# Kernel optimization log

Hardware: AMD Instinct MI355X
Metric: run time of the kernel (lower is better)

The kernel has to match this reference:

```python
import jax, jax.numpy as jnp
import numpy as np

B = 1
H_IMG, W_IMG = 64, 64
NF = H_IMG * W_IMG          # 4096 front/query tokens
NS = 1024                   # satellite tokens (32x32 grid)
SAT_IN, FRONT_IN = 768, 320
NH, HD = 8, 64
MD = NH * HD                # 512
GHID, GHD = 128, 16
GMD = NH * GHD              # 128
GEO_RATIO, ROPE_BASE = 0.5, 10000.0
LAMBDA_GEO, LAMBDA_GEOM = 1.0, 1.0
EPS = 1e-5


def _linear(x, w, b):
    return x @ w.T + b


def _layernorm(x, g, b):
    m = x.mean(-1, keepdims=True)
    v = jnp.var(x, axis=-1, keepdims=True)
    return (x - m) / jnp.sqrt(v + EPS) * g + b


def _georope(t, xy):
    """Continuous 2D (x,y) rotary embedding on the first GEO_RATIO fraction of head_dim.
    t: [B,NH,N,HD], xy: [B,N,2]."""
    rot = int(HD * GEO_RATIO)       # rotated dims (32)
    axis = rot // 2                 # dims per spatial axis (16)
    half = axis // 2                # frequency pairs per axis (8)
    inv_freq = ROPE_BASE ** (-jnp.arange(half, dtype=t.dtype) / half)

    def rot_axis(a, coord):
        th = coord[:, None, :, None] * inv_freq   # [B,1,N,half]
        c, s = jnp.cos(th), jnp.sin(th)
        a1, a2 = a[..., :half], a[..., half:]
        return jnp.concatenate([a1 * c - a2 * s, a1 * s + a2 * c], axis=-1)

    tx = rot_axis(t[..., :axis], xy[..., 0])
    ty = rot_axis(t[..., axis:rot], xy[..., 1])
    return jnp.concatenate([tx, ty, t[..., rot:]], axis=-1)


def _heads(x, hd):
    b, n, _ = x.shape
    return x.reshape(b, n, NH, hd).transpose(0, 2, 1, 3)


def setup_inputs() -> dict:
    key = jax.random.key(0)
    ks = iter(jax.random.split(key, 64))

    def w(*shape):
        return jax.random.normal(next(ks), shape, jnp.float32) / np.sqrt(shape[-1]).astype(np.float32)

    z = lambda n: jnp.zeros((n,), jnp.float32)
    o = lambda n: jnp.ones((n,), jnp.float32)
    return {
        "front_feat": jax.random.normal(next(ks), (B, FRONT_IN, H_IMG, W_IMG), jnp.float32),
        "front_bev_xy": jax.random.uniform(next(ks), (B, NF, 2), jnp.float32, -1.0, 1.0),
        "sat_tokens": jax.random.normal(next(ks), (B, NS, SAT_IN), jnp.float32),
        "sat_xy": jax.random.uniform(next(ks), (B, NS, 2), jnp.float32, -1.0, 1.0),
        "front_plucker": jax.random.normal(next(ks), (B, NF, 6), jnp.float32),
        "pos_w1": w(MD, 2), "pos_b1": z(MD), "pos_w2": w(MD, MD), "pos_b2": z(MD),
        "fa_w": w(MD, FRONT_IN), "fa_b": z(MD), "fa_ln_g": o(MD), "fa_ln_b": z(MD),
        "qn_g": o(MD), "qn_b": z(MD),
        "sa_w": w(MD, SAT_IN), "sa_b": z(MD), "sa_ln_g": o(MD), "sa_ln_b": z(MD),
        "wq": w(MD, MD), "bq": z(MD), "wk": w(MD, MD), "bk": z(MD), "wv": w(MD, MD), "bv": z(MD),
        "plk_w1": w(GHID, 6), "plk_b1": z(GHID), "plk_w2": w(GHID, GHID), "plk_b2": z(GHID),
        "sxy_w1": w(GHID, 2), "sxy_b1": z(GHID), "sxy_w2": w(GHID, GHID), "sxy_b2": z(GHID),
        "gqn_g": o(GHID), "gqn_b": z(GHID), "gkn_g": o(GHID), "gkn_b": z(GHID),
        "wqg": w(GMD, GHID), "bqg": z(GMD), "wkg": w(GMD, GHID), "bkg": z(GMD),
    }


def reference(front_feat, front_bev_xy, sat_tokens, sat_xy, front_plucker,
              pos_w1, pos_b1, pos_w2, pos_b2, fa_w, fa_b, fa_ln_g, fa_ln_b,
              qn_g, qn_b, sa_w, sa_b, sa_ln_g, sa_ln_b, wq, bq, wk, bk, wv, bv,
              plk_w1, plk_b1, plk_w2, plk_b2, sxy_w1, sxy_b1, sxy_w2, sxy_b2,
              gqn_g, gqn_b, gkn_g, gkn_b, wqg, bqg, wkg, bkg):
    b = front_feat.shape[0]
    ff = front_feat.reshape(b, FRONT_IN, NF).transpose(0, 2, 1)      # [B,NF,C]
    pos = _linear(jax.nn.silu(_linear(front_bev_xy, pos_w1, pos_b1)), pos_w2, pos_b2)
    feat = _layernorm(_linear(ff, fa_w, fa_b), fa_ln_g, fa_ln_b)
    q_embed = _layernorm(pos + feat, qn_g, qn_b)
    sat_feat = _layernorm(_linear(sat_tokens, sa_w, sa_b), sa_ln_g, sa_ln_b)
    q = _heads(_linear(q_embed, wq, bq), HD)                         # [B,H,NF,HD]
    k = _heads(_linear(sat_feat, wk, bk), HD)                        # [B,H,NS,HD]
    v = _heads(_linear(sat_feat, wv, bv), HD)
    qr = _georope(q, front_bev_xy)
    kr = _georope(k, sat_xy)
    logits = jnp.einsum('bhqd,bhkd->bhqk', qr, kr) / np.float32(np.sqrt(HD))
    # learned geometric Q/K stream (Plucker rays vs sat xy)
    plk = _layernorm(_linear(jax.nn.silu(_linear(front_plucker, plk_w1, plk_b1)), plk_w2, plk_b2), gqn_g, gqn_b)
    sgf = _layernorm(_linear(jax.nn.silu(_linear(sat_xy, sxy_w1, sxy_b1)), sxy_w2, sxy_b2), gkn_g, gkn_b)
    qg = _heads(_linear(plk, wqg, bqg), GHD)
    kg = _heads(_linear(sgf, wkg, bkg), GHD)
    logits = logits + LAMBDA_GEOM * (jnp.einsum('bhqd,bhkd->bhqk', qg, kg) / np.float32(np.sqrt(GHD)))
    # additive pairwise squared-distance bias, broadcast over heads
    dist2 = ((front_bev_xy[:, :, None, :] - sat_xy[:, None, :, :]) ** 2).sum(-1)   # [B,NF,NS]
    logits = logits - LAMBDA_GEO * dist2[:, None]
    attn = jax.nn.softmax(logits, axis=-1)
    read = jnp.einsum('bhqk,bhkd->bhqd', attn, v)
    return read.transpose(0, 2, 1, 3).reshape(b, NF, MD)
```

## Files before the change

kernel.cpp:

```cpp
#include <hip/hip_runtime.h>
#include <hip/hip_bf16.h>
#include <stdint.h>

#define NF 4096
#define NS 1024
#define MD 512
#define HD 64
#define DA 96
#define GHID 128

#define L2E 1.44269504f
#define S2L 1.6986436f
#define SMAX 12.0f

typedef unsigned short u16;
typedef __attribute__((ext_vector_type(8))) short bf8v;
typedef __attribute__((ext_vector_type(4))) float f4v;

__device__ __forceinline__ u16 f2bf(float f) {
  __hip_bfloat16 h = __float2bfloat16(f);
  return __builtin_bit_cast(u16, h);
}
__device__ __forceinline__ float bf2f(u16 u) {
  union { unsigned u; float f; } v; v.u = ((unsigned)u) << 16; return v.f;
}
__device__ __forceinline__ f4v mfma16(bf8v a, bf8v b, f4v c) {
  return __builtin_amdgcn_mfma_f32_16x16x32_bf16(a, b, c, 0, 0, 0);
}
__device__ __forceinline__ void gld16(const void* g, void* l) {
  __builtin_amdgcn_global_load_lds(
      (const __attribute__((address_space(1))) unsigned int*)g,
      (__attribute__((address_space(3))) unsigned int*)l, 16, 0, 0);
}

#define OFF_POSW2 0
#define OFF_FAW   262144
#define OFF_SAW   425984
#define OFF_WQ    819200
#define OFF_WKV   1081344
#define OFF_PLKW2 1605632
#define OFF_SXYW2 1622016
#define OFF_WQG   1638400
#define OFF_WKG   1654784
#define OFF_SATT  1671168
#define TOTW      2457600

#define EPI_OUT  0
#define EPI_ROPE 1
#define EPI_VT   2
#define EPI_GEO  3

__global__ __launch_bounds__(256) void k_l0(
    const float* __restrict__ s0, const float* __restrict__ s1,
    const float* __restrict__ s2, const float* __restrict__ s3,
    const float* __restrict__ s4, const float* __restrict__ s5,
    const float* __restrict__ s6, const float* __restrict__ s7,
    const float* __restrict__ s8, const float* __restrict__ s9,
    const float* __restrict__ s10, u16* __restrict__ pool,
    const float* __restrict__ bk, const float* __restrict__ bv,
    float* __restrict__ bkv,
    const float* __restrict__ ff, u16* __restrict__ ffT,
    const float* __restrict__ in0, const float* __restrict__ w0,
    const float* __restrict__ b0, u16* __restrict__ o0,
    const float* __restrict__ in1, const float* __restrict__ w1,
    const float* __restrict__ b1, u16* __restrict__ o1,
    const float* __restrict__ in2, const float* __restrict__ w2,
    const float* __restrict__ b2, u16* __restrict__ o2,
    u16* __restrict__ Qaug, u16* __restrict__ Kaug, float* __restrict__ kk2) {
  __shared__ u16 sT[32][72];
  int blk = blockIdx.x, t = threadIdx.x;
  if (blk < 2401) {
    int i4 = blk * 256 + t;
    if (i4 < TOTW / 4) {
      int idx = i4 * 4;
      const float* src; int off;
      if      (idx < OFF_FAW)   { src = s0;  off = OFF_POSW2; }
      else if (idx < OFF_SAW)   { src = s1;  off = OFF_FAW; }
      else if (idx < OFF_WQ)    { src = s2;  off = OFF_SAW; }
      else if (idx < OFF_WKV)   { src = s3;  off = OFF_WQ; }
      else if (idx < 1343488)   { src = s4;  off = OFF_WKV; }
      else if (idx < OFF_PLKW2) { src = s5;  off = 1343488; }
      else if (idx < OFF_SXYW2) { src = s6;  off = OFF_PLKW2; }
      else if (idx < OFF_WQG)   { src = s7;  off = OFF_SXYW2; }
      else if (idx < OFF_WKG)   { src = s8;  off = OFF_WQG; }
      else if (idx < OFF_SATT)  { src = s9;  off = OFF_WKG; }
      else                      { src = s10; off = OFF_SATT; }
      float4 v = *(const float4*)(src + (idx - off));
      ushort4 o;
      o.x = f2bf(v.x); o.y = f2bf(v.y); o.z = f2bf(v.z); o.w = f2bf(v.w);
      *(ushort4*)(pool + idx) = o;
    } else if (i4 < TOTW / 4 + 256) {
      int j = (i4 - TOTW / 4) * 4;
#pragma unroll
      for (int e = 0; e < 4; ++e) {
        int b = j + e;
        bkv[b] = (b < 512) ? bk[b] : bv[b - 512];
      }
    }
  } else if (blk < 3041) {
    int lb = blk - 2401;
    int n0 = (lb & 63) * 64, c0 = (lb >> 6) * 32;
    {
      int cr = t >> 3, nc = (t & 7) * 8;
      const float* src = ff + (size_t)(c0 + cr) * NF + n0 + nc;
      float4 v0 = *(const float4*)src, v1 = *(const float4*)(src + 4);
      bf8v p;
      p[0]=(short)f2bf(v0.x); p[1]=(short)f2bf(v0.y); p[2]=(short)f2bf(v0.z); p[3]=(short)f2bf(v0.w);
      p[4]=(short)f2bf(v1.x); p[5]=(short)f2bf(v1.y); p[6]=(short)f2bf(v1.z); p[7]=(short)f2bf(v1.w);
      *(bf8v*)&sT[cr][nc] = p;
    }
    __syncthreads();
    {
      int r = t >> 2, cc = (t & 3) * 8;
      bf8v p;
#pragma unroll
      for (int e = 0; e < 8; ++e) p[e] = (short)sT[cc + e][r];
      *(bf8v*)(ffT + (size_t)(n0 + r) * 320 + c0 + cc) = p;
    }
  } else if (blk < 13793) {
    int lb = blk - 3041;
    const float *in, *w, *b; u16* o; int mlog, K, idx;
    if (lb < 8192)       { in = in0; w = w0; b = b0; o = o0; mlog = 9; K = 2; idx = lb * 256 + t; }
    else if (lb < 10240) { in = in1; w = w1; b = b1; o = o1; mlog = 7; K = 6; idx = (lb - 8192) * 256 + t; }
    else                 { in = in2; w = w2; b = b2; o = o2; mlog = 7; K = 2; idx = (lb - 10240) * 256 + t; }
    int M = 1 << mlog;
    int n = idx >> mlog, m = idx & (M - 1);
    float acc = b[m];
    for (int k = 0; k < K; ++k) acc += in[n * K + k] * w[m * K + k];
    o[idx] = f2bf(acc / (1.f + __expf(-acc)));
  } else {
    int id = (blk - 13793) * 256 + t;
    int side = id >= NF * 8;
    int lid = side ? id - NF * 8 : id;
    int n = lid >> 3, h = lid & 7;
    const float* xy = side ? in2 : in0;
    u16* aug = side ? Kaug : Qaug;
    int nrows = side ? NS : NF;
    float x = xy[n * 2], y = xy[n * 2 + 1];
    bf8v p0, z;
#pragma unroll
    for (int e = 0; e < 8; ++e) { p0[e] = 0; z[e] = 0; }
    p0[0] = (short)f2bf(S2L * x);
    p0[1] = (short)f2bf(S2L * y);
    u16* dst = aug + ((size_t)h * nrows + n) * DA + 80;
    *(bf8v*)dst = p0;
    *(bf8v*)(dst + 8) = z;
    if (side && h == 0) kk2[n] = L2E * (x * x + y * y) + SMAX;
  }
}

__device__ __forceinline__ void gemm_body128(const u16* __restrict__ A, const u16* __restrict__ W,
                                             const float* __restrict__ bias, u16* __restrict__ out,
                                             int m0, int n0, int N, int K) {
  __shared__ u16 sA[2][128 * 64];
  __shared__ u16 sB[2][64 * 64];
  const int tid = threadIdx.x, w = tid >> 6, lane = tid & 63;
  const int l16 = lane & 15, lh = lane >> 4;

  f4v acc[2][4];
#pragma unroll
  for (int m = 0; m < 2; ++m)
#pragma unroll
    for (int j = 0; j < 4; ++j) acc[m][j] = (f4v){0.f, 0.f, 0.f, 0.f};

  auto stageA = [&](int buf, int k0) {
#pragma unroll
    for (int i = 0; i < 4; ++i) {
      int c = i * 256 + tid;
      int row = c >> 3, cp = c & 7;
      int sc_ = cp ^ (row & 7);
      gld16(A + (size_t)(m0 + row) * K + k0 + sc_ * 8, &sA[buf][c * 8]);
    }
  };
  auto stageB = [&](int buf, int k0) {
#pragma unroll
    for (int i = 0; i < 2; ++i) {
      int c = i * 256 + tid;
      int row = c >> 3, cp = c & 7;
      int sc_ = cp ^ (row & 7);
      gld16(W + (size_t)(n0 + row) * K + k0 + sc_ * 8, &sB[buf][c * 8]);
    }
  };

  stageA(0, 0); stageB(0, 0);
  __syncthreads();
  const int NK = K >> 6;
  for (int ks = 0; ks < NK; ++ks) {
    int nb = ks & 1;
    if (ks + 1 < NK) { stageA(nb ^ 1, (ks + 1) * 64); stageB(nb ^ 1, (ks + 1) * 64); }
#pragma unroll
    for (int kk = 0; kk < 2; ++kk) {
      bf8v af[2], bfr[4];
#pragma unroll
      for (int m = 0; m < 2; ++m) {
        int row = w * 32 + m * 16 + l16;
        int cp = (kk * 4 + lh) ^ (row & 7);
        af[m] = *(const bf8v*)&sA[nb][row * 64 + cp * 8];
      }
#pragma unroll
      for (int j = 0; j < 4; ++j) {
        int row = j * 16 + l16;
        int cp = (kk * 4 + lh) ^ (row & 7);
        bfr[j] = *(const bf8v*)&sB[nb][row * 64 + cp * 8];
      }
#pragma unroll
      for (int m = 0; m < 2; ++m)
#pragma unroll
        for (int j = 0; j < 4; ++j) acc[m][j] = mfma16(af[m], bfr[j], acc[m][j]);
    }
    __syncthreads();
  }
#pragma unroll
  for (int m = 0; m < 2; ++m) {
    int grow = m0 + w * 32 + m * 16 + (lh << 2);
#pragma unroll
    for (int j = 0; j < 4; ++j) {
      int gcol = n0 + j * 16 + l16;
      float bvs = bias ? bias[gcol] : 0.f;
#pragma unroll
      for (int r = 0; r < 4; ++r)
        out[(size_t)(grow + r) * N + gcol] = f2bf(acc[m][j][r] + bvs);
    }
  }
}

__device__ __forceinline__ void gemm_body(const u16* __restrict__ A, const u16* __restrict__ W,
                                          const float* __restrict__ bias, u16* __restrict__ out,
                                          int m0, int n0, int N, int K,
                                          int mode, float scale, const float* __restrict__ xy,
                                          u16* __restrict__ aug, int nrows) {
  constexpr int MR = 2, NR = 2;
  __shared__ u16 sA[2][64 * 64];
  __shared__ u16 sB[2][64 * 64];
  const int tid = threadIdx.x, w = tid >> 6, lane = tid & 63;
  const int l16 = lane & 15, lh = lane >> 4;
  const int wr = w >> 1, wc = w & 1;

  f4v acc[MR][NR];
#pragma unroll
  for (int m = 0; m < MR; ++m)
#pragma unroll
    for (int j = 0; j < NR; ++j) acc[m][j] = (f4v){0.f, 0.f, 0.f, 0.f};

  auto stageA = [&](int buf, int k0) {
#pragma unroll
    for (int i = 0; i < 2; ++i) {
      int c = i * 256 + tid;
      int row = c >> 3, cp = c & 7;
      int sc_ = cp ^ (row & 7);
      gld16(A + (size_t)(m0 + row) * K + k0 + sc_ * 8, &sA[buf][c * 8]);
    }
  };
  auto stageB = [&](int buf, int k0) {
#pragma unroll
    for (int i = 0; i < 2; ++i) {
      int c = i * 256 + tid;
      int row = c >> 3, cp = c & 7;
      int sc_ = cp ^ (row & 7);
      gld16(W + (size_t)(n0 + row) * K + k0 + sc_ * 8, &sB[buf][c * 8]);
    }
  };

  stageA(0, 0); stageB(0, 0);
  __syncthreads();
  const int NK = K >> 6;
  for (int ks = 0; ks < NK; ++ks) {
    int nb = ks & 1;
    if (ks + 1 < NK) { stageA(nb ^ 1, (ks + 1) * 64); stageB(nb ^ 1, (ks + 1) * 64); }
#pragma unroll
    for (int kk = 0; kk < 2; ++kk) {
      bf8v af[MR], bfr[NR];
#pragma unroll
      for (int m = 0; m < MR; ++m) {
        int row = wr * 32 + m * 16 + l16;
        int cp = (kk * 4 + lh) ^ (row & 7);
        af[m] = *(const bf8v*)&sA[nb][row * 64 + cp * 8];
      }
#pragma unroll
      for (int j = 0; j < NR; ++j) {
        int row = wc * 32 + j * 16 + l16;
        int cp = (kk * 4 + lh) ^ (row & 7);
        bfr[j] = *(const bf8v*)&sB[nb][row * 64 + cp * 8];
      }
#pragma unroll
      for (int m = 0; m < MR; ++m)
#pragma unroll
        for (int j = 0; j < NR; ++j) acc[m][j] = mfma16(af[m], bfr[j], acc[m][j]);
    }
    __syncthreads();
  }

  if (mode == EPI_OUT) {
#pragma unroll
    for (int m = 0; m < MR; ++m) {
      int grow = m0 + wr * 32 + m * 16 + (lh << 2);
#pragma unroll
      for (int j = 0; j < NR; ++j) {
        int gcol = n0 + wc * 32 + j * 16 + l16;
        float bvs = bias ? bias[gcol] : 0.f;
#pragma unroll
        for (int r = 0; r < 4; ++r)
          out[(size_t)(grow + r) * N + gcol] = f2bf(acc[m][j][r] + bvs);
      }
    }
  } else if (mode == EPI_ROPE) {
    float fr = __expf(-(float)(l16 & 7) * 1.1512925465f);
#pragma unroll
    for (int m = 0; m < MR; ++m) {
      int grow = m0 + wr * 32 + m * 16 + (lh << 2);
#pragma unroll
      for (int j = 0; j < NR; ++j) {
        int gcol = n0 + wc * 32 + j * 16 + l16;
        int h = gcol >> 6, d = gcol & 63;
        float bvs = bias[gcol];
#pragma unroll
        for (int r = 0; r < 4; ++r) {
          int n = grow + r;
          float val = acc[m][j][r] + bvs;
          float part = __shfl_xor(val, 8);
          float outv = val;
          if (wc == 0) {
            float2 c2 = ((const float2*)xy)[n];
            float coord = j ? c2.y : c2.x;
            float sn, cs;
            __sincosf(coord * fr, &sn, &cs);
            outv = (l16 & 8) ? (part * sn + val * cs) : (val * cs - part * sn);
          }
          aug[((size_t)h * nrows + n) * DA + d] = f2bf(outv * scale);
        }
      }
    }
  } else if (mode == EPI_VT) {
#pragma unroll
    for (int m = 0; m < MR; ++m) {
      int grow = m0 + wr * 32 + m * 16 + (lh << 2);
#pragma unroll
      for (int j = 0; j < NR; ++j) {
        int gcol = n0 + wc * 32 + j * 16 + l16;
        int vcol = gcol - 512;
        int h = vcol >> 6, d = vcol & 63;
        float bvs = bias[gcol];
        ushort4 o;
        o.x = f2bf(acc[m][j][0] + bvs);
        o.y = f2bf(acc[m][j][1] + bvs);
        o.z = f2bf(acc[m][j][2] + bvs);
        o.w = f2bf(acc[m][j][3] + bvs);
        *(ushort4*)(aug + ((size_t)(h * 64 + d)) * NS + grow) = o;
      }
    }
  } else {
#pragma unroll
    for (int m = 0; m < MR; ++m) {
      int grow = m0 + wr * 32 + m * 16 + (lh << 2);
#pragma unroll
      for (int j = 0; j < NR; ++j) {
        int gcol = n0 + wc * 32 + j * 16 + l16;
        int h = gcol >> 4, dg = gcol & 15;
        float bvs = bias[gcol];
#pragma unroll
        for (int r = 0; r < 4; ++r)
          aug[((size_t)h * nrows + grow + r) * DA + 64 + dg] = f2bf((acc[m][j][r] + bvs) * scale);
      }
    }
  }
}

struct GP { const u16* A; const u16* W; const float* bias; u16* out;
            int K; int N; int M; int mode; float scale; const float* xy;
            u16* aug; int nrows; };

__device__ __forceinline__ void gemm_dispatch128(const GP& g, int blk) {
  int mt = g.M >> 7;
  int m0 = (blk % mt) * 128, n0 = (blk / mt) * 64;
  gemm_body128(g.A, g.W, g.bias, g.out, m0, n0, g.N, g.K);
}
__device__ __forceinline__ void gemm_dispatch(const GP& g, int blk) {
  int mt = g.M >> 6;
  int m0 = (blk % mt) * 64, n0 = (blk / mt) * 64;
  gemm_body(g.A, g.W, g.bias, g.out, m0, n0, g.N, g.K,
            g.mode, g.scale, g.xy, g.aug, g.nrows);
}

__global__ __launch_bounds__(256) void k_gemm_L1(GP a, GP b, GP c, GP d, GP e) {
  int blk = blockIdx.x;
  if (blk < 256)       gemm_dispatch128(a, blk);
  else if (blk < 512)  gemm_dispatch128(b, blk - 256);
  else if (blk < 576)  gemm_dispatch128(c, blk - 512);
  else if (blk < 640)  gemm_dispatch128(d, blk - 576);
  else                 gemm_dispatch128(e, blk - 640);
}
__global__ __launch_bounds__(256) void k_gemm_L2(GP a, GP b, GP c, GP d, u16* VTp) {
  int blk = blockIdx.x;
  if (blk < 512) {
    gemm_dispatch(a, blk);
  } else if (blk < 768) {
    int lb = blk - 512;
    int m0 = (lb & 15) * 64, n0 = (lb >> 4) * 64;
    if (n0 >= 512)
      gemm_body(b.A, b.W, b.bias, b.out, m0, n0, b.N, b.K, EPI_VT, 1.f, nullptr, VTp, NS);
    else
      gemm_body(b.A, b.W, b.bias, b.out, m0, n0, b.N, b.K, b.mode, b.scale, b.xy, b.aug, b.nrows);
  } else if (blk < 896) {
    gemm_dispatch(c, blk - 768);
  } else {
    gemm_dispatch(d, blk - 896);
  }
}

__global__ __launch_bounds__(256) void k_ln_all(
    const u16* __restrict__ feat_pre, const u16* __restrict__ pos,
    const float* __restrict__ fg, const float* __restrict__ fb,
    const float* __restrict__ qg, const float* __restrict__ qb2,
    u16* __restrict__ q_embed,
    const u16* __restrict__ satf_pre, const float* __restrict__ sg,
    const float* __restrict__ sb, u16* __restrict__ satf,
    const u16* __restrict__ ginq, const u16* __restrict__ gink,
    const float* __restrict__ ggq, const float* __restrict__ gbq,
    const float* __restrict__ ggk, const float* __restrict__ gbk,
    u16* __restrict__ goutq, u16* __restrict__ goutk) {
  int blk = blockIdx.x;
  int w = threadIdx.x >> 6, lane = threadIdx.x & 63;
  if (blk < 1024) {
    int row = blk * 4 + w;
    bf8v v = *(const bf8v*)(feat_pre + (size_t)row * 512 + lane * 8);
    float x[8];
#pragma unroll
    for (int e = 0; e < 8; ++e) x[e] = bf2f((u16)v[e]);
    float s = 0.f, q = 0.f;
#pragma unroll
    for (int e = 0; e < 8; ++e) { s += x[e]; q += x[e] * x[e]; }
#pragma unroll
    for (int mm = 1; mm < 64; mm <<= 1) { s += __shfl_xor(s, mm); q += __shfl_xor(q, mm); }
    float mean = s / 512.f, var = q / 512.f - mean * mean;
    float rstd = rsqrtf(var + 1e-5f);
    bf8v vp = *(const bf8v*)(pos + (size_t)row * 512 + lane * 8);
#pragma unroll
    for (int e = 0; e < 8; ++e)
      x[e] = (x[e] - mean) * rstd * fg[lane * 8 + e] + fb[lane * 8 + e] + bf2f((u16)vp[e]);
    s = 0.f; q = 0.f;
#pragma unroll
    for (int e = 0; e < 8; ++e) { s += x[e]; q += x[e] * x[e]; }
#pragma unroll
    for (int mm = 1; mm < 64; mm <<= 1) { s += __shfl_xor(s, mm); q += __shfl_xor(q, mm); }
    mean = s / 512.f; var = q / 512.f - mean * mean;
    rstd = rsqrtf(var + 1e-5f);
    bf8v ov;
#pragma unroll
    for (int e = 0; e < 8; ++e)
      ov[e] = (short)f2bf((x[e] - mean) * rstd * qg[lane * 8 + e] + qb2[lane * 8 + e]);
    *(bf8v*)(q_embed + (size_t)row * 512 + lane * 8) = ov;
  } else if (blk < 1280) {
    int row = (blk - 1024) * 4 + w;
    bf8v v = *(const bf8v*)(satf_pre + (size_t)row * 512 + lane * 8);
    float x[8];
#pragma unroll
    for (int e = 0; e < 8; ++e) x[e] = bf2f((u16)v[e]);
    float s = 0.f, q = 0.f;
#pragma unroll
    for (int e = 0; e < 8; ++e) { s += x[e]; q += x[e] * x[e]; }
#pragma unroll
    for (int mm = 1; mm < 64; mm <<= 1) { s += __shfl_xor(s, mm); q += __shfl_xor(q, mm); }
    float mean = s / 512.f, var = q / 512.f - mean * mean;
    float rstd = rsqrtf(var + 1e-5f);
    bf8v ov;
#pragma unroll
    for (int e = 0; e < 8; ++e)
      ov[e] = (short)f2bf((x[e] - mean) * rstd * sg[lane * 8 + e] + sb[lane * 8 + e]);
    *(bf8v*)(satf + (size_t)row * 512 + lane * 8) = ov;
  } else {
    int row = (blk - 1280) * 4 + w;
    const u16* in; const float *g, *b; u16* out;
    if (row < 4096) { in = ginq; g = ggq; b = gbq; out = goutq; }
    else { row -= 4096; in = gink; g = ggk; b = gbk; out = goutk; }
    uint32_t v = *(const uint32_t*)(in + (size_t)row * 128 + lane * 2);
    float x0 = bf2f((u16)(v & 0xffff)), x1 = bf2f((u16)(v >> 16));
    float s = x0 + x1, q = x0 * x0 + x1 * x1;
#pragma unroll
    for (int mm = 1; mm < 64; mm <<= 1) { s += __shfl_xor(s, mm); q += __shfl_xor(q, mm); }
    float mean = s / 128.f, var = q / 128.f - mean * mean;
    float rstd = rsqrtf(var + 1e-5f);
    u16 o0 = f2bf((x0 - mean) * rstd * g[lane * 2] + b[lane * 2]);
    u16 o1 = f2bf((x1 - mean) * rstd * g[lane * 2 + 1] + b[lane * 2 + 1]);
    *(uint32_t*)(out + (size_t)row * 128 + lane * 2) = (uint32_t)o0 | ((uint32_t)o1 << 16);
  }
}

__global__ __launch_bounds__(256, 5) void k_flash(const u16* __restrict__ Qa,
                                                  const u16* __restrict__ Ka,
                                                  const u16* __restrict__ VT,
                                                  const float* __restrict__ kk2,
                                                  u16* __restrict__ Opart,
                                                  float* __restrict__ lbuf) {
  const int h = blockIdx.y, qb = blockIdx.x, sp = blockIdx.z;
  const int tid = threadIdx.x, w = tid >> 6, lane = tid & 63;
  const int l16 = lane & 15, lh = lane >> 4;
  __shared__ u16 sK[64][100];
  __shared__ u16 sV[64][68];
  __shared__ u16 sP[4][16][68];
  __shared__ float sKK[512];

  ((float2*)sKK)[tid] = ((const float2*)(kk2 + sp * 512))[tid];

  const int qrow = qb * 64 + w * 16 + l16;
  bf8v qf[3];
#pragma unroll
  for (int c = 0; c < 3; ++c)
    qf[c] = *(const bf8v*)(Qa + (size_t)(h * NF + qrow) * DA + c * 32 + lh * 8);

  bf8v ONES;
#pragma unroll
  for (int i = 0; i < 8; ++i) ONES[i] = (short)0x3F80;

  const int crow = qb * 64 + w * 16 + (lh << 2);
  float l_run[4] = {0.f, 0.f, 0.f, 0.f};
  f4v accO[4];
#pragma unroll
  for (int d = 0; d < 4; ++d) accO[d] = (f4v){0.f, 0.f, 0.f, 0.f};

  const int kt0 = sp * 8;
  bf8v kreg[3], vreg[2];
  auto sload = [&](int t8) {
    int kb = (kt0 + t8) * 64;
#pragma unroll
    for (int i = 0; i < 3; ++i) {
      int c = tid + i * 256; int r = c / 12, off = (c % 12) * 8;
      kreg[i] = *(const bf8v*)(Ka + ((size_t)(h * NS) + kb + r) * DA + off);
    }
#pragma unroll
    for (int i = 0; i < 2; ++i) {
      int c = tid + i * 256; int d = c >> 3, off = (c & 7) * 8;
      vreg[i] = *(const bf8v*)(VT + ((size_t)(h * HD) + d) * NS + kb + off);
    }
  };
  auto swrite = [&]() {
#pragma unroll
    for (int i = 0; i < 3; ++i) {
      int c = tid + i * 256; int r = c / 12, off = (c % 12) * 8;
      *(bf8v*)&sK[r][off] = kreg[i];
    }
#pragma unroll
    for (int i = 0; i < 2; ++i) {
      int c = tid + i * 256; int d = c >> 3, off = (c & 7) * 8;
      *(bf8v*)&sV[d][off] = vreg[i];
    }
  };

  sload(0); swrite();
  __syncthreads();
  for (int t8 = 0; t8 < 8; ++t8) {
    if (t8 < 7) sload(t8 + 1);
#pragma unroll
    for (int j = 0; j < 4; ++j) {
      f4v s4 = (f4v){0.f, 0.f, 0.f, 0.f};
#pragma unroll
      for (int c = 0; c < 3; ++c) {
        bf8v kf = *(const bf8v*)&sK[j * 16 + l16][c * 32 + lh * 8];
        s4 = mfma16(qf[c], kf, s4);
      }
      float ck = sKK[t8 * 64 + j * 16 + l16];
#pragma unroll
      for (int r = 0; r < 4; ++r) {
        float pv = exp2f(s4[r] - ck);
        sP[w][(lh << 2) + r][j * 16 + l16] = f2bf(pv);
      }
    }
    bf8v pf0 = *(const bf8v*)&sP[w][l16][lh * 8];
    bf8v pf1 = *(const bf8v*)&sP[w][l16][32 + lh * 8];
    f4v ls = (f4v){0.f, 0.f, 0.f, 0.f};
    ls = mfma16(pf0, ONES, ls);
    ls = mfma16(pf1, ONES, ls);
#pragma unroll
    for (int r = 0; r < 4; ++r) l_run[r] += ls[r];
#pragma unroll
    for (int c = 0; c < 2; ++c) {
      bf8v pf = (c == 0) ? pf0 : pf1;
#pragma unroll
      for (int d = 0; d < 4; ++d) {
        bf8v vf = *(const bf8v*)&sV[d * 16 + l16][c * 32 + lh * 8];
        accO[d] = mfma16(pf, vf, accO[d]);
      }
    }
    __syncthreads();
    if (t8 < 7) swrite();
    __syncthreads();
  }
  size_t obase = (size_t)(sp * 8 + h) * NF + crow;
#pragma unroll
  for (int d = 0; d < 4; ++d)
#pragma unroll
    for (int r = 0; r < 4; ++r)
      Opart[(obase + r) * 64 + d * 16 + l16] = f2bf(accO[d][r]);
  if (l16 == 0) {
#pragma unroll
    for (int r = 0; r < 4; ++r) lbuf[obase + r] = l_run[r];
  }
}

__global__ void k_combine(const u16* __restrict__ Opart, const float* __restrict__ lbuf,
                          float* __restrict__ out) {
  int i4 = blockIdx.x * 256 + threadIdx.x;
  int n = i4 >> 7;
  int c4 = i4 & 127, h = c4 >> 4, d4 = c4 & 15;
  float l = lbuf[(size_t)h * NF + n] + lbuf[(size_t)(8 + h) * NF + n];
  float rl = 1.f / l;
  ushort4 a = ((const ushort4*)(Opart + ((size_t)h * NF + n) * 64))[d4];
  ushort4 b = ((const ushort4*)(Opart + ((size_t)(8 + h) * NF + n) * 64))[d4];
  float4 r;
  r.x = (bf2f(a.x) + bf2f(b.x)) * rl;
  r.y = (bf2f(a.y) + bf2f(b.y)) * rl;
  r.z = (bf2f(a.z) + bf2f(b.z)) * rl;
  r.w = (bf2f(a.w) + bf2f(b.w)) * rl;
  ((float4*)out)[i4] = r;
}

extern "C" void kernel_launch(void* const* d_in, const int* in_sizes, int n_in,
                              void* d_out, int out_size, void* d_ws, size_t ws_size,
                              hipStream_t stream) {
  (void)in_sizes; (void)n_in; (void)out_size; (void)ws_size;
  const float* front_feat = (const float*)d_in[0];
  const float* bev_xy     = (const float*)d_in[1];
  const float* sat_tokens = (const float*)d_in[2];
  const float* sat_xy     = (const float*)d_in[3];
  const float* plucker    = (const float*)d_in[4];
  const float* pos_w1 = (const float*)d_in[5];
  const float* pos_b1 = (const float*)d_in[6];
  const float* pos_w2 = (const float*)d_in[7];
  const float* pos_b2 = (const float*)d_in[8];
  const float* fa_w   = (const float*)d_in[9];
  const float* fa_b   = (const float*)d_in[10];
  const float* fa_ln_g = (const float*)d_in[11];
  const float* fa_ln_b = (const float*)d_in[12];
  const float* qn_g   = (const float*)d_in[13];
  const float* qn_b   = (const float*)d_in[14];
  const float* sa_w   = (const float*)d_in[15];
  const float* sa_b   = (const float*)d_in[16];
  const float* sa_ln_g = (const float*)d_in[17];
  const float* sa_ln_b = (const float*)d_in[18];
  const float* wq = (const float*)d_in[19];
  const float* bq = (const float*)d_in[20];
  const float* wk = (const float*)d_in[21];
  const float* bk = (const float*)d_in[22];
  const float* wv = (const float*)d_in[23];
  const float* bv = (const float*)d_in[24];
  const float* plk_w1 = (const float*)d_in[25];
  const float* plk_b1 = (const float*)d_in[26];
  const float* plk_w2 = (const float*)d_in[27];
  const float* plk_b2 = (const float*)d_in[28];
  const float* sxy_w1 = (const float*)d_in[29];
  const float* sxy_b1 = (const float*)d_in[30];
  const float* sxy_w2 = (const float*)d_in[31];
  const float* sxy_b2 = (const float*)d_in[32];
  const float* gqn_g = (const float*)d_in[33];
  const float* gqn_b = (const float*)d_in[34];
  const float* gkn_g = (const float*)d_in[35];
  const float* gkn_b = (const float*)d_in[36];
  const float* wqg = (const float*)d_in[37];
  const float* bqg = (const float*)d_in[38];
  const float* wkg = (const float*)d_in[39];
  const float* bkg = (const float*)d_in[40];

  char* ws = (char*)d_ws;
  size_t off = 0;
  auto alloc = [&](size_t bytes) {
    size_t r = off;
    off += (bytes + 255) & ~(size_t)255;
    return r;
  };
  u16*   wpool   = (u16*)(ws + alloc((size_t)TOTW * 2));
  float* bkv     = (float*)(ws + alloc(1024 * 4));
  u16*   ffT     = (u16*)(ws + alloc((size_t)NF * 320 * 2));
  u16*   pos_h   = (u16*)(ws + alloc((size_t)NF * MD * 2));
  u16*   plk_h   = (u16*)(ws + alloc((size_t)NF * GHID * 2));
  u16*   sxy_h   = (u16*)(ws + alloc((size_t)NS * GHID * 2));
  u16*   pos     = (u16*)(ws + alloc((size_t)NF * MD * 2));
  u16*   feat_pre= (u16*)(ws + alloc((size_t)NF * MD * 2));
  u16*   satf_pre= (u16*)(ws + alloc((size_t)NS * MD * 2));
  u16*   satf    = (u16*)(ws + alloc((size_t)NS * MD * 2));
  u16*   q_embed = (u16*)(ws + alloc((size_t)NF * MD * 2));
  u16*   plk2    = (u16*)(ws + alloc((size_t)NF * GHID * 2));
  u16*   sxy2    = (u16*)(ws + alloc((size_t)NS * GHID * 2));
  u16*   Qaug    = (u16*)(ws + alloc((size_t)8 * NF * DA * 2));
  u16*   Kaug    = (u16*)(ws + alloc((size_t)8 * NS * DA * 2));
  u16*   VT      = (u16*)(ws + alloc((size_t)8 * HD * NS * 2));
  float* kk2     = (float*)(ws + alloc((size_t)NS * 4));
  u16*   Opart   = (u16*)(ws + alloc((size_t)2 * 8 * NF * 64 * 2));
  float* lbuf    = (float*)(ws + alloc((size_t)2 * 8 * NF * 4));
  u16* plk_ln = plk_h;
  u16* sgf    = sxy_h;

  dim3 b256(256);
  k_l0<<<dim3(13953), b256, 0, stream>>>(
      pos_w2, fa_w, sa_w, wq, wk, wv, plk_w2, sxy_w2, wqg, wkg, sat_tokens,
      wpool, bk, bv, bkv, front_feat, ffT,
      bev_xy, pos_w1, pos_b1, pos_h,
      plucker, plk_w1, plk_b1, plk_h,
      sat_xy, sxy_w1, sxy_b1, sxy_h,
      Qaug, Kaug, kk2);

  GP gpos {pos_h, wpool + OFF_POSW2, pos_b2, pos, 512, 512, 4096, EPI_OUT, 0.f, nullptr, nullptr, 0};
  GP gfeat{ffT, wpool + OFF_FAW, fa_b, feat_pre, 320, 512, 4096, EPI_OUT, 0.f, nullptr, nullptr, 0};
  GP gsat {wpool + OFF_SATT, wpool + OFF_SAW, sa_b, satf_pre, 768, 512, 1024, EPI_OUT, 0.f, nullptr, nullptr, 0};
  GP ggq1 {plk_h, wpool + OFF_PLKW2, plk_b2, plk2, 128, 128, 4096, EPI_OUT, 0.f, nullptr, nullptr, 0};
  GP ggk1 {sxy_h, wpool + OFF_SXYW2, sxy_b2, sxy2, 128, 128, 1024, EPI_OUT, 0.f, nullptr, nullptr, 0};
  k_gemm_L1<<<dim3(656), b256, 0, stream>>>(gpos, gfeat, gsat, ggq1, ggk1);

  k_ln_all<<<dim3(2560), b256, 0, stream>>>(
      feat_pre, pos, fa_ln_g, fa_ln_b, qn_g, qn_b, q_embed,
      satf_pre, sa_ln_g, sa_ln_b, satf,
      plk2, sxy2, gqn_g, gqn_b, gkn_g, gkn_b, plk_ln, sgf);

  GP gq  {q_embed, wpool + OFF_WQ, bq, nullptr, 512, 512, 4096, EPI_ROPE, 0.125f * L2E, bev_xy, Qaug, NF};
  GP gkv {satf, wpool + OFF_WKV, bkv, nullptr, 512, 1024, 1024, EPI_ROPE, 1.f, sat_xy, Kaug, NS};
  GP ggq2{plk_ln, wpool + OFF_WQG, bqg, nullptr, 128, 128, 4096, EPI_GEO, 0.25f * L2E, nullptr, Qaug, NF};
  GP ggk2{sgf, wpool + OFF_WKG, bkg, nullptr, 128, 128, 1024, EPI_GEO, 1.f, nullptr, Kaug, NS};
  k_gemm_L2<<<dim3(928), b256, 0, stream>>>(gq, gkv, ggq2, ggk2, VT);

  k_flash<<<dim3(NF / 64, 8, 2), b256, 0, stream>>>(Qaug, Kaug, VT, kk2, Opart, lbuf);
  k_combine<<<dim3(NF * MD / 4 / 256), b256, 0, stream>>>(Opart, lbuf, (float*)d_out);
}
```

Before: 79.25 us.

## Split flash attention keys four ways and fuse combine via last-block atomic

Raises the key-dimension split of the flash kernel from 2 to 4, so the grid grows from 1024 to 2048 blocks for better occupancy across CUs. It also removes the separate combine kernel: each block bumps an atomic counter per (head, query block), and the last finisher sums the partial outputs and normalises them into the final output. Flags are zeroed in the first kernel. The cost is more partial-output traffic, a serial tail in the winning block, and reliance on threadfence and acquire-release atomics for correctness.

```diff
diff --git a/kernel.cpp b/kernel.cpp
--- a/kernel.cpp
+++ b/kernel.cpp
@@ -12,6 +12,7 @@
 #define L2E 1.44269504f
 #define S2L 1.6986436f
 #define SMAX 12.0f
+#define NSPLIT 4
 
 typedef unsigned short u16;
 typedef __attribute__((ext_vector_type(8))) short bf8v;
@@ -66,7 +67,8 @@
     const float* __restrict__ b1, u16* __restrict__ o1,
     const float* __restrict__ in2, const float* __restrict__ w2,
     const float* __restrict__ b2, u16* __restrict__ o2,
-    u16* __restrict__ Qaug, u16* __restrict__ Kaug, float* __restrict__ kk2) {
+    u16* __restrict__ Qaug, u16* __restrict__ Kaug, float* __restrict__ kk2,
+    int* __restrict__ flags) {
   __shared__ u16 sT[32][72];
   int blk = blockIdx.x, t = threadIdx.x;
   if (blk < 2401) {
@@ -130,6 +132,7 @@
     o[idx] = f2bf(acc / (1.f + __expf(-acc)));
   } else {
     int id = (blk - 13793) * 256 + t;
+    if (id < 512) flags[id] = 0;
     int side = id >= NF * 8;
     int lid = side ? id - NF * 8 : id;
     int n = lid >> 3, h = lid & 7;
@@ -490,16 +493,19 @@
                                                   const u16* __restrict__ VT,
                                                   const float* __restrict__ kk2,
                                                   u16* __restrict__ Opart,
-                                                  float* __restrict__ lbuf) {
+                                                  float* __restrict__ lbuf,
+                                                  int* __restrict__ flags,
+                                                  float* __restrict__ out) {
   const int h = blockIdx.y, qb = blockIdx.x, sp = blockIdx.z;
   const int tid = threadIdx.x, w = tid >> 6, lane = tid & 63;
   const int l16 = lane & 15, lh = lane >> 4;
   __shared__ u16 sK[64][100];
   __shared__ u16 sV[64][68];
   __shared__ u16 sP[4][16][68];
-  __shared__ float sKK[512];
-
-  ((float2*)sKK)[tid] = ((const float2*)(kk2 + sp * 512))[tid];
+  __shared__ float sKK[256];
+  __shared__ int sWin;
+
+  if (tid < 64) ((float4*)sKK)[tid] = ((const float4*)(kk2 + sp * 256))[tid];
 
   const int qrow = qb * 64 + w * 16 + l16;
   bf8v qf[3];
@@ -517,7 +523,7 @@
 #pragma unroll
   for (int d = 0; d < 4; ++d) accO[d] = (f4v){0.f, 0.f, 0.f, 0.f};
 
-  const int kt0 = sp * 8;
+  const int kt0 = sp * (NS / 64 / NSPLIT);
   bf8v kreg[3], vreg[2];
   auto sload = [&](int t8) {
     int kb = (kt0 + t8) * 64;
@@ -547,8 +553,9 @@
 
   sload(0); swrite();
   __syncthreads();
-  for (int t8 = 0; t8 < 8; ++t8) {
-    if (t8 < 7) sload(t8 + 1);
+  const int NT = NS / 64 / NSPLIT;
+  for (int t8 = 0; t8 < NT; ++t8) {
+    if (t8 < NT - 1) sload(t8 + 1);
 #pragma unroll
     for (int j = 0; j < 4; ++j) {
       f4v s4 = (f4v){0.f, 0.f, 0.f, 0.f};
@@ -581,7 +588,7 @@
       }
     }
     __syncthreads();
-    if (t8 < 7) swrite();
+    if (t8 < NT - 1) swrite();
     __syncthreads();
   }
   size_t obase = (size_t)(sp * 8 + h) * NF + crow;
@@ -594,23 +601,34 @@
 #pragma unroll
     for (int r = 0; r < 4; ++r) lbuf[obase + r] = l_run[r];
   }
-}
-
-__global__ void k_combine(const u16* __restrict__ Opart, const float* __restrict__ lbuf,
-                          float* __restrict__ out) {
-  int i4 = blockIdx.x * 256 + threadIdx.x;
-  int n = i4 >> 7;
-  int c4 = i4 & 127, h = c4 >> 4, d4 = c4 & 15;
-  float l = lbuf[(size_t)h * NF + n] + lbuf[(size_t)(8 + h) * NF + n];
-  float rl = 1.f / l;
-  ushort4 a = ((const ushort4*)(Opart + ((size_t)h * NF + n) * 64))[d4];
-  ushort4 b = ((const ushort4*)(Opart + ((size_t)(8 + h) * NF + n) * 64))[d4];
-  float4 r;
-  r.x = (bf2f(a.x) + bf2f(b.x)) * rl;
-  r.y = (bf2f(a.y) + bf2f(b.y)) * rl;
-  r.z = (bf2f(a.z) + bf2f(b.z)) * rl;
-  r.w = (bf2f(a.w) + bf2f(b.w)) * rl;
-  ((float4*)out)[i4] = r;
+
+  if (tid == 0) {
+    __threadfence();
+    int old = __hip_atomic_fetch_add(&flags[h * 64 + qb], 1,
+                                     __ATOMIC_ACQ_REL, __HIP_MEMORY_SCOPE_AGENT);
+    sWin = (old == NSPLIT - 1);
+  }
+  __syncthreads();
+  if (sWin) {
+#pragma unroll
+    for (int it = 0; it < 4; ++it) {
+      int idx = it * 256 + tid;
+      int rn = idx >> 4, d4 = idx & 15;
+      int n = qb * 64 + rn;
+      float l = 0.f;
+      float ox = 0.f, oy = 0.f, oz = 0.f, ow = 0.f;
+#pragma unroll
+      for (int s2 = 0; s2 < NSPLIT; ++s2) {
+        size_t base = (size_t)(s2 * 8 + h) * NF + n;
+        l += lbuf[base];
+        ushort4 a = ((const ushort4*)(Opart + base * 64))[d4];
+        ox += bf2f(a.x); oy += bf2f(a.y); oz += bf2f(a.z); ow += bf2f(a.w);
+      }
+      float rl = 1.f / l;
+      float4 r = make_float4(ox * rl, oy * rl, oz * rl, ow * rl);
+      ((float4*)out)[(size_t)n * 128 + h * 16 + d4] = r;
+    }
+  }
 }
 
 extern "C" void kernel_launch(void* const* d_in, const int* in_sizes, int n_in,
@@ -683,8 +701,9 @@
   u16*   Kaug    = (u16*)(ws + alloc((size_t)8 * NS * DA * 2));
   u16*   VT      = (u16*)(ws + alloc((size_t)8 * HD * NS * 2));
   float* kk2     = (float*)(ws + alloc((size_t)NS * 4));
-  u16*   Opart   = (u16*)(ws + alloc((size_t)2 * 8 * NF * 64 * 2));
-  float* lbuf    = (float*)(ws + alloc((size_t)2 * 8 * NF * 4));
+  u16*   Opart   = (u16*)(ws + alloc((size_t)NSPLIT * 8 * NF * 64 * 2));
+  float* lbuf    = (float*)(ws + alloc((size_t)NSPLIT * 8 * NF * 4));
+  int*   flags   = (int*)(ws + alloc(512 * 4));
   u16* plk_ln = plk_h;
   u16* sgf    = sxy_h;
 
@@ -695,7 +714,7 @@
       bev_xy, pos_w1, pos_b1, pos_h,
       plucker, plk_w1, plk_b1, plk_h,
       sat_xy, sxy_w1, sxy_b1, sxy_h,
-      Qaug, Kaug, kk2);
+      Qaug, Kaug, kk2, flags);
 
   GP gpos {pos_h, wpool + OFF_POSW2, pos_b2, pos, 512, 512, 4096, EPI_OUT, 0.f, nullptr, nullptr, 0};
   GP gfeat{ffT, wpool + OFF_FAW, fa_b, feat_pre, 320, 512, 4096, EPI_OUT, 0.f, nullptr, nullptr, 0};
@@ -715,6 +734,6 @@
   GP ggk2{sgf, wpool + OFF_WKG, bkg, nullptr, 128, 128, 1024, EPI_GEO, 1.f, nullptr, Kaug, NS};
   k_gemm_L2<<<dim3(928), b256, 0, stream>>>(gq, gkv, ggq2, ggk2, VT);
 
-  k_flash<<<dim3(NF / 64, 8, 2), b256, 0, stream>>>(Qaug, Kaug, VT, kk2, Opart, lbuf);
-  k_combine<<<dim3(NF * MD / 4 / 256), b256, 0, stream>>>(Opart, lbuf, (float*)d_out);
-}
+  k_flash<<<dim3(NF / 64, 8, NSPLIT), b256, 0, stream>>>(Qaug, Kaug, VT, kk2,
+                                                         Opart, lbuf, flags, (float*)d_out);
+}
```

Measured after the change: 242.5 us. 3.06x slower.
